# Kernel tuning notes

Hardware: AMD Instinct MI355X
Metric: run time of the kernel (lower is better)

Reference implementation:

```python
import jax, jax.numpy as jnp
import numpy as np

BATCH = 65536
SEQ_LEN = 32
EMB = 64
H = 128


def setup_inputs() -> dict:
    key = jax.random.key(0)
    ks = jax.random.split(key, 12)
    s = 0.05
    inp = {
        "last_pos": jax.random.normal(ks[0], (BATCH, 2), jnp.float32),
        "last_pos_rel": jax.random.normal(ks[1], (BATCH, 2), jnp.float32),
        "hh": jax.random.normal(ks[2], (1, BATCH, H), jnp.float32),
        "ch": jax.random.normal(ks[3], (1, BATCH, H), jnp.float32),
        "seq_start_end": jnp.sort(jax.random.randint(ks[4], (256, 2), 0, BATCH), axis=0),
        # LSTM(embedding_dim -> h_dim), PyTorch gate order [i, f, g, o]
        "w_ih": jax.random.normal(ks[5], (4 * H, EMB), jnp.float32) * s,
        "w_hh": jax.random.normal(ks[6], (4 * H, H), jnp.float32) * s,
        "b_ih": jax.random.normal(ks[7], (4 * H,), jnp.float32) * s,
        "b_hh": jax.random.normal(ks[8], (4 * H,), jnp.float32) * s,
        # spatial_embedding: Linear(2 -> EMB)
        "w_emb": jax.random.normal(ks[9], (EMB, 2), jnp.float32) * s,
        "b_emb": jax.random.normal(ks[10], (EMB,), jnp.float32) * s,
        # hidden2pos: Linear(H -> 2)
        "w_pos": jax.random.normal(ks[11], (2, H), jnp.float32) * s,
        "b_pos": jnp.zeros((2,), jnp.float32),
    }
    return inp


def _decode(last_pos, last_pos_rel, hh, ch, w_ih, w_hh, b_ih, b_hh,
            w_emb, b_emb, w_pos, b_pos):
    h0, c0 = hh[0], ch[0]                      # (B, H)
    x0 = last_pos_rel @ w_emb.T + b_emb        # (B, EMB)
    b = b_ih + b_hh

    def step(carry, _):
        h, c, lp, x = carry
        gates = x @ w_ih.T + h @ w_hh.T + b    # (B, 4H)
        i, f, g, o = jnp.split(gates, 4, axis=-1)
        c2 = jax.nn.sigmoid(f) * c + jax.nn.sigmoid(i) * jnp.tanh(g)
        h2 = jax.nn.sigmoid(o) * jnp.tanh(c2)
        rel = h2 @ w_pos.T + b_pos             # (B, 2)
        cur = rel + lp
        x2 = rel @ w_emb.T + b_emb             # next decoder input embedding
        return (h2, c2, cur, x2), rel

    (hN, cN, _, _), rels = jax.lax.scan(step, (h0, c0, last_pos, x0),
                                        None, length=SEQ_LEN)
    # rels: (SEQ_LEN, B, 2) == pred_traj_fake_rel; hN[None]: (1, B, H)
    return rels, hN[None]


def reference(last_pos, last_pos_rel, hh, ch, seq_start_end,
              w_ih, w_hh, b_ih, b_hh, w_emb, b_emb, w_pos, b_pos):
    # seq_start_end is unused when pool_every_timestep=False
    return _decode(last_pos, last_pos_rel, hh, ch,
                   w_ih, w_hh, b_ih, b_hh, w_emb, b_emb, w_pos, b_pos)
```

## Files before the change

kernel.cpp:

```cpp
#include <hip/hip_runtime.h>

#define B_TOT 65536
#define SEQ   32

typedef __bf16 bf16_8 __attribute__((ext_vector_type(8)));
typedef float  float4v __attribute__((ext_vector_type(4)));

__device__ inline float bf2f(unsigned short s){
    unsigned u = ((unsigned)s) << 16;
    return __builtin_bit_cast(float, u);
}
__device__ inline unsigned short f2bf(float f){
    unsigned u = __builtin_bit_cast(unsigned, f);
    u += 0x7FFFu + ((u >> 16) & 1u);
    return (unsigned short)(u >> 16);
}
__device__ inline float fsig(float x){
    float e = __builtin_amdgcn_exp2f(-1.4426950408889634f * x);
    return __builtin_amdgcn_rcpf(1.0f + e);
}
__device__ inline float ftanh(float x){
    float e = __builtin_amdgcn_exp2f(-2.8853900817779268f * x);
    return 2.0f * __builtin_amdgcn_rcpf(1.0f + e) - 1.0f;
}

__global__ void prep_kernel(const float* __restrict__ w_ih,
                            const float* __restrict__ w_hh,
                            const float* __restrict__ b_ih,
                            const float* __restrict__ b_hh,
                            const float* __restrict__ w_emb,
                            const float* __restrict__ b_emb,
                            const float* __restrict__ w_pos,
                            const float* __restrict__ b_pos,
                            unsigned short* __restrict__ weff,
                            float* __restrict__ beff,
                            float* __restrict__ m2,
                            unsigned short* __restrict__ wposb)
{
    int n = threadIdx.x;
    float m20 = 0.f, m21 = 0.f, bi = 0.f;
    for (int e = 0; e < 64; ++e){
        float wv = w_ih[n*64 + e];
        m20 += w_emb[e*2 + 0] * wv;
        m21 += w_emb[e*2 + 1] * wv;
        bi  += b_emb[e] * wv;
    }
    m2[n]       = m20;
    m2[512 + n] = m21;
    beff[n] = b_ih[n] + b_hh[n] + bi + b_pos[0]*m20 + b_pos[1]*m21;
    for (int k = 0; k < 128; ++k){
        float wv = w_hh[n*128 + k] + w_pos[k]*m20 + w_pos[128 + k]*m21;
        weff[n*128 + k] = f2bf(wv);
    }
    if (n < 256) wposb[n] = f2bf(w_pos[n]);
}

__global__ __launch_bounds__(256, 2) void dec_kernel(
    const float* __restrict__ lpr,
    const float* __restrict__ hh,
    const float* __restrict__ ch,
    const float* __restrict__ b_pos,
    const unsigned short* __restrict__ wposb,
    const unsigned short* __restrict__ weff,
    const float* __restrict__ beff,
    const float* __restrict__ m2,
    float* __restrict__ out)
{
    __shared__ __align__(16) unsigned short lh[2][16][136];
    __shared__ float ubuf[16][2];

    const int tid  = threadIdx.x;
    const int w    = tid >> 6;
    const int lane = tid & 63;
    const int q    = lane >> 4;
    const int l    = lane & 15;
    const int row0 = blockIdx.x << 4;

    {
        int r = tid >> 4, c8 = (tid & 15) << 3;
        const float* ph = hh + ((row0 + r) << 7) + c8;
        const float* pc = ch + ((row0 + r) << 7) + c8;
        float4 h0v = *(const float4*)ph, h1v = *(const float4*)(ph + 4);
        float4 c0v = *(const float4*)pc, c1v = *(const float4*)(pc + 4);
        unsigned short hb[8], cb[8];
        hb[0]=f2bf(h0v.x); hb[1]=f2bf(h0v.y); hb[2]=f2bf(h0v.z); hb[3]=f2bf(h0v.w);
        hb[4]=f2bf(h1v.x); hb[5]=f2bf(h1v.y); hb[6]=f2bf(h1v.z); hb[7]=f2bf(h1v.w);
        cb[0]=f2bf(c0v.x); cb[1]=f2bf(c0v.y); cb[2]=f2bf(c0v.z); cb[3]=f2bf(c0v.w);
        cb[4]=f2bf(c1v.x); cb[5]=f2bf(c1v.y); cb[6]=f2bf(c1v.z); cb[7]=f2bf(c1v.w);
        *(uint4*)&lh[0][r][c8] = *(const uint4*)hb;
        *(uint4*)&lh[1][r][c8] = *(const uint4*)cb;
    }
    __syncthreads();

    float c0r[4], c1r[4];
#pragma unroll
    for (int r4 = 0; r4 < 4; ++r4){
        c0r[r4] = bf2f(lh[1][q*4 + r4][32*w + l]);
        c1r[r4] = bf2f(lh[1][q*4 + r4][32*w + 16 + l]);
    }

    bf16_8 a[4];
#pragma unroll
    for (int kt = 0; kt < 4; ++kt)
        a[kt] = *(const bf16_8*)&lh[0][l][kt*32 + q*8];

    bf16_8 bfr[8][4];
    float bias[8];
#pragma unroll
    for (int t8 = 0; t8 < 8; ++t8){
        int nb = ((t8 >> 1) << 7) + 32*w + ((t8 & 1) << 4) + l;
#pragma unroll
        for (int kt = 0; kt < 4; ++kt)
            bfr[t8][kt] = *(const bf16_8*)(weff + (nb << 7) + kt*32 + q*8);
        bias[t8] = beff[nb];
    }

    bf16_8 wp[4];
    {
        int n2 = (l < 2) ? l : 0;
#pragma unroll
        for (int kt = 0; kt < 4; ++kt)
            wp[kt] = *(const bf16_8*)(wposb + (n2 << 7) + kt*32 + q*8);
    }
    float bposv = b_pos[l & 1];

    if (w == 0){
        float4v racc = {0.f, 0.f, 0.f, 0.f};
#pragma unroll
        for (int kt = 0; kt < 4; ++kt)
            racc = __builtin_amdgcn_mfma_f32_16x16x32_bf16(a[kt], wp[kt], racc, 0, 0, 0);
        if (l < 2){
#pragma unroll
            for (int r4 = 0; r4 < 4; ++r4){
                int row = q*4 + r4;
                float lp = lpr[((row0 + row) << 1) + l];
                ubuf[row][l] = lp - (racc[r4] + bposv);
            }
        }
    }
    __syncthreads();

    float4v acc[8];

    auto do_gates = [&](){
#pragma unroll
        for (int t8 = 0; t8 < 8; ++t8){
            float bb = bias[t8];
            acc[t8] = (float4v){bb, bb, bb, bb};
        }
#pragma unroll
        for (int kt = 0; kt < 4; ++kt)
#pragma unroll
            for (int t8 = 0; t8 < 8; ++t8)
                acc[t8] = __builtin_amdgcn_mfma_f32_16x16x32_bf16(a[kt], bfr[t8][kt], acc[t8], 0, 0, 0);
    };

    auto do_elem_write = [&](int buf, int final_h){
#pragma unroll
        for (int X = 0; X < 2; ++X){
#pragma unroll
            for (int r4 = 0; r4 < 4; ++r4){
                float ig = acc[0 + X][r4];
                float fg = acc[2 + X][r4];
                float gg = acc[4 + X][r4];
                float og = acc[6 + X][r4];
                float cold = X ? c1r[r4] : c0r[r4];
                float c2 = fsig(fg)*cold + fsig(ig)*ftanh(gg);
                float h2 = fsig(og)*ftanh(c2);
                if (X) c1r[r4] = c2; else c0r[r4] = c2;
                lh[buf][q*4 + r4][32*w + 16*X + l] = f2bf(h2);
                if (final_h)
                    out[SEQ*B_TOT*2 + ((row0 + q*4 + r4) << 7) + 32*w + 16*X + l] = h2;
            }
        }
    };

    auto reload_and_rel = [&](int buf, int t){
#pragma unroll
        for (int kt = 0; kt < 4; ++kt)
            a[kt] = *(const bf16_8*)&lh[buf][l][kt*32 + q*8];
        if (w == 0){
            float4v racc = {0.f, 0.f, 0.f, 0.f};
#pragma unroll
            for (int kt = 0; kt < 4; ++kt)
                racc = __builtin_amdgcn_mfma_f32_16x16x32_bf16(a[kt], wp[kt], racc, 0, 0, 0);
            if (l < 2){
#pragma unroll
                for (int r4 = 0; r4 < 4; ++r4)
                    out[t*(B_TOT*2) + ((row0 + q*4 + r4) << 1) + l] = racc[r4] + bposv;
            }
        }
    };

    do_gates();
    {
        float uu0[4], uu1[4];
#pragma unroll
        for (int r4 = 0; r4 < 4; ++r4){
            uu0[r4] = ubuf[q*4 + r4][0];
            uu1[r4] = ubuf[q*4 + r4][1];
        }
#pragma unroll
        for (int t8 = 0; t8 < 8; ++t8){
            int nb = ((t8 >> 1) << 7) + 32*w + ((t8 & 1) << 4) + l;
            float ma = m2[nb], mb = m2[512 + nb];
#pragma unroll
            for (int r4 = 0; r4 < 4; ++r4)
                acc[t8][r4] += uu0[r4]*ma + uu1[r4]*mb;
        }
    }
    do_elem_write(1, 0);
    __syncthreads();
    reload_and_rel(1, 0);

    for (int t = 1; t < SEQ; ++t){
        do_gates();
        do_elem_write((t + 1) & 1, t == SEQ - 1);
        __syncthreads();
        reload_and_rel((t + 1) & 1, t);
    }
}

extern "C" void kernel_launch(void* const* d_in, const int* in_sizes, int n_in,
                              void* d_out, int out_size, void* d_ws, size_t ws_size,
                              hipStream_t stream)
{
    (void)in_sizes; (void)n_in; (void)out_size; (void)ws_size;

    const float* lpr   = (const float*)d_in[1];
    const float* hh    = (const float*)d_in[2];
    const float* ch    = (const float*)d_in[3];
    const float* w_ih  = (const float*)d_in[5];
    const float* w_hh  = (const float*)d_in[6];
    const float* b_ih  = (const float*)d_in[7];
    const float* b_hh  = (const float*)d_in[8];
    const float* w_emb = (const float*)d_in[9];
    const float* b_emb = (const float*)d_in[10];
    const float* w_pos = (const float*)d_in[11];
    const float* b_pos = (const float*)d_in[12];

    unsigned short* weff  = (unsigned short*)d_ws;
    float* beff           = (float*)((char*)d_ws + 512*128*2);
    float* m2             = (float*)((char*)d_ws + 512*128*2 + 2048);
    unsigned short* wposb = (unsigned short*)((char*)d_ws + 512*128*2 + 2048 + 4096);

    hipLaunchKernelGGL(prep_kernel, dim3(1), dim3(512), 0, stream,
                       w_ih, w_hh, b_ih, b_hh, w_emb, b_emb, w_pos, b_pos,
                       weff, beff, m2, wposb);
    hipLaunchKernelGGL(dec_kernel, dim3(B_TOT/16), dim3(256), 0, stream,
                       lpr, hh, ch, b_pos, wposb, weff, beff, m2,
                       (float*)d_out);
}
```

Measured before the change: 549.2 us.

## Transpose MFMA operands so gates are computed as W·hᵀ with vectorized state I/O

Swaps the MFMA operand roles so weights are the A operand and the hidden state is the B operand. Each lane then owns four consecutive gate outputs for one batch row, which allows vectorized bf16x4 LDS writes of h, float4 reads of c and final h, and bias loaded as a float4 accumulator init. The initial LDS staging of h/c and the extra barrier are removed, and the hidden2pos projection rotates across waves per timestep instead of always running on wave 0. The w_pos buffer is zero-padded to 16 rows to serve as the MFMA A operand.

```diff
diff --git a/kernel.cpp b/kernel.cpp
--- a/kernel.cpp
+++ b/kernel.cpp
@@ -4,12 +4,10 @@
 #define SEQ   32
 
 typedef __bf16 bf16_8 __attribute__((ext_vector_type(8)));
+typedef __bf16 bf16_4 __attribute__((ext_vector_type(4)));
 typedef float  float4v __attribute__((ext_vector_type(4)));
-
-__device__ inline float bf2f(unsigned short s){
-    unsigned u = ((unsigned)s) << 16;
-    return __builtin_bit_cast(float, u);
-}
+typedef float  float2v __attribute__((ext_vector_type(2)));
+
 __device__ inline unsigned short f2bf(float f){
     unsigned u = __builtin_bit_cast(unsigned, f);
     u += 0x7FFFu + ((u >> 16) & 1u);
@@ -35,7 +33,7 @@
                             unsigned short* __restrict__ weff,
                             float* __restrict__ beff,
                             float* __restrict__ m2,
-                            unsigned short* __restrict__ wposb)
+                            unsigned short* __restrict__ wposA)
 {
     int n = threadIdx.x;
     float m20 = 0.f, m21 = 0.f, bi = 0.f;
@@ -52,7 +50,8 @@
         float wv = w_hh[n*128 + k] + w_pos[k]*m20 + w_pos[128 + k]*m21;
         weff[n*128 + k] = f2bf(wv);
     }
-    if (n < 256) wposb[n] = f2bf(w_pos[n]);
+    if (n < 256) wposA[n] = f2bf(w_pos[n]);
+    for (int idx = n; idx < 14*128; idx += 512) wposA[256 + idx] = 0;
 }
 
 __global__ __launch_bounds__(256, 2) void dec_kernel(
@@ -60,7 +59,7 @@
     const float* __restrict__ hh,
     const float* __restrict__ ch,
     const float* __restrict__ b_pos,
-    const unsigned short* __restrict__ wposb,
+    const unsigned short* __restrict__ wposA,
     const unsigned short* __restrict__ weff,
     const float* __restrict__ beff,
     const float* __restrict__ m2,
@@ -75,141 +74,124 @@
     const int q    = lane >> 4;
     const int l    = lane & 15;
     const int row0 = blockIdx.x << 4;
-
-    {
-        int r = tid >> 4, c8 = (tid & 15) << 3;
-        const float* ph = hh + ((row0 + r) << 7) + c8;
-        const float* pc = ch + ((row0 + r) << 7) + c8;
-        float4 h0v = *(const float4*)ph, h1v = *(const float4*)(ph + 4);
-        float4 c0v = *(const float4*)pc, c1v = *(const float4*)(pc + 4);
-        unsigned short hb[8], cb[8];
-        hb[0]=f2bf(h0v.x); hb[1]=f2bf(h0v.y); hb[2]=f2bf(h0v.z); hb[3]=f2bf(h0v.w);
-        hb[4]=f2bf(h1v.x); hb[5]=f2bf(h1v.y); hb[6]=f2bf(h1v.z); hb[7]=f2bf(h1v.w);
-        cb[0]=f2bf(c0v.x); cb[1]=f2bf(c0v.y); cb[2]=f2bf(c0v.z); cb[3]=f2bf(c0v.w);
-        cb[4]=f2bf(c1v.x); cb[5]=f2bf(c1v.y); cb[6]=f2bf(c1v.z); cb[7]=f2bf(c1v.w);
-        *(uint4*)&lh[0][r][c8] = *(const uint4*)hb;
-        *(uint4*)&lh[1][r][c8] = *(const uint4*)cb;
+    const int batch = row0 + l;
+
+    bf16_8 wA[8][4];
+    float4v bias4[8];
+#pragma unroll
+    for (int t8 = 0; t8 < 8; ++t8){
+        int nbase = ((t8 >> 1) << 7) + 32*w + ((t8 & 1) << 4);
+        int gA = nbase + l;
+#pragma unroll
+        for (int kt = 0; kt < 4; ++kt)
+            wA[t8][kt] = *(const bf16_8*)(weff + (gA << 7) + kt*32 + (q << 3));
+        bias4[t8] = *(const float4v*)(beff + nbase + (q << 2));
+    }
+
+    bf16_8 wpA[4];
+#pragma unroll
+    for (int kt = 0; kt < 4; ++kt)
+        wpA[kt] = *(const bf16_8*)(wposA + (l << 7) + kt*32 + (q << 3));
+    const float bp0 = b_pos[0], bp1 = b_pos[1];
+
+    float4v cst[2];
+#pragma unroll
+    for (int X = 0; X < 2; ++X)
+        cst[X] = *(const float4v*)(ch + (batch << 7) + 32*w + 16*X + (q << 2));
+
+    bf16_8 b[4];
+#pragma unroll
+    for (int kt = 0; kt < 4; ++kt){
+        const float* ph = hh + (batch << 7) + kt*32 + (q << 3);
+        float4v h0 = *(const float4v*)ph;
+        float4v h1 = *(const float4v*)(ph + 4);
+        bf16_8 t;
+        t[0]=(__bf16)h0[0]; t[1]=(__bf16)h0[1]; t[2]=(__bf16)h0[2]; t[3]=(__bf16)h0[3];
+        t[4]=(__bf16)h1[0]; t[5]=(__bf16)h1[1]; t[6]=(__bf16)h1[2]; t[7]=(__bf16)h1[3];
+        b[kt] = t;
+    }
+
+    if (w == 0){
+        float4v r = {0.f, 0.f, 0.f, 0.f};
+#pragma unroll
+        for (int kt = 0; kt < 4; ++kt)
+            r = __builtin_amdgcn_mfma_f32_16x16x32_bf16(wpA[kt], b[kt], r, 0, 0, 0);
+        if (q == 0){
+            float2v lp = *(const float2v*)(lpr + (batch << 1));
+            ubuf[l][0] = lp[0] - (r[0] + bp0);
+            ubuf[l][1] = lp[1] - (r[1] + bp1);
+        }
     }
     __syncthreads();
 
-    float c0r[4], c1r[4];
-#pragma unroll
-    for (int r4 = 0; r4 < 4; ++r4){
-        c0r[r4] = bf2f(lh[1][q*4 + r4][32*w + l]);
-        c1r[r4] = bf2f(lh[1][q*4 + r4][32*w + 16 + l]);
-    }
-
-    bf16_8 a[4];
-#pragma unroll
-    for (int kt = 0; kt < 4; ++kt)
-        a[kt] = *(const bf16_8*)&lh[0][l][kt*32 + q*8];
-
-    bf16_8 bfr[8][4];
-    float bias[8];
-#pragma unroll
-    for (int t8 = 0; t8 < 8; ++t8){
-        int nb = ((t8 >> 1) << 7) + 32*w + ((t8 & 1) << 4) + l;
-#pragma unroll
-        for (int kt = 0; kt < 4; ++kt)
-            bfr[t8][kt] = *(const bf16_8*)(weff + (nb << 7) + kt*32 + q*8);
-        bias[t8] = beff[nb];
-    }
-
-    bf16_8 wp[4];
-    {
-        int n2 = (l < 2) ? l : 0;
-#pragma unroll
-        for (int kt = 0; kt < 4; ++kt)
-            wp[kt] = *(const bf16_8*)(wposb + (n2 << 7) + kt*32 + q*8);
-    }
-    float bposv = b_pos[l & 1];
-
-    if (w == 0){
-        float4v racc = {0.f, 0.f, 0.f, 0.f};
-#pragma unroll
-        for (int kt = 0; kt < 4; ++kt)
-            racc = __builtin_amdgcn_mfma_f32_16x16x32_bf16(a[kt], wp[kt], racc, 0, 0, 0);
-        if (l < 2){
-#pragma unroll
-            for (int r4 = 0; r4 < 4; ++r4){
-                int row = q*4 + r4;
-                float lp = lpr[((row0 + row) << 1) + l];
-                ubuf[row][l] = lp - (racc[r4] + bposv);
-            }
-        }
-    }
-    __syncthreads();
-
     float4v acc[8];
 
     auto do_gates = [&](){
 #pragma unroll
-        for (int t8 = 0; t8 < 8; ++t8){
-            float bb = bias[t8];
-            acc[t8] = (float4v){bb, bb, bb, bb};
-        }
-#pragma unroll
-        for (int kt = 0; kt < 4; ++kt)
+        for (int t8 = 0; t8 < 8; ++t8)
+            acc[t8] = __builtin_amdgcn_mfma_f32_16x16x32_bf16(wA[t8][0], b[0], bias4[t8], 0, 0, 0);
+#pragma unroll
+        for (int kt = 1; kt < 4; ++kt)
 #pragma unroll
             for (int t8 = 0; t8 < 8; ++t8)
-                acc[t8] = __builtin_amdgcn_mfma_f32_16x16x32_bf16(a[kt], bfr[t8][kt], acc[t8], 0, 0, 0);
+                acc[t8] = __builtin_amdgcn_mfma_f32_16x16x32_bf16(wA[t8][kt], b[kt], acc[t8], 0, 0, 0);
     };
 
-    auto do_elem_write = [&](int buf, int final_h){
+    auto do_elem_write = [&](int buf, bool finalh){
 #pragma unroll
         for (int X = 0; X < 2; ++X){
+            bf16_4 hv;
+            float4v hf;
 #pragma unroll
             for (int r4 = 0; r4 < 4; ++r4){
                 float ig = acc[0 + X][r4];
                 float fg = acc[2 + X][r4];
                 float gg = acc[4 + X][r4];
                 float og = acc[6 + X][r4];
-                float cold = X ? c1r[r4] : c0r[r4];
-                float c2 = fsig(fg)*cold + fsig(ig)*ftanh(gg);
+                float c2 = fsig(fg)*cst[X][r4] + fsig(ig)*ftanh(gg);
                 float h2 = fsig(og)*ftanh(c2);
-                if (X) c1r[r4] = c2; else c0r[r4] = c2;
-                lh[buf][q*4 + r4][32*w + 16*X + l] = f2bf(h2);
-                if (final_h)
-                    out[SEQ*B_TOT*2 + ((row0 + q*4 + r4) << 7) + 32*w + 16*X + l] = h2;
+                cst[X][r4] = c2;
+                hv[r4] = (__bf16)h2;
+                hf[r4] = h2;
             }
+            *(bf16_4*)&lh[buf][l][32*w + 16*X + (q << 2)] = hv;
+            if (finalh)
+                *(float4v*)(out + SEQ*B_TOT*2 + (batch << 7) + 32*w + 16*X + (q << 2)) = hf;
         }
     };
 
     auto reload_and_rel = [&](int buf, int t){
 #pragma unroll
         for (int kt = 0; kt < 4; ++kt)
-            a[kt] = *(const bf16_8*)&lh[buf][l][kt*32 + q*8];
-        if (w == 0){
-            float4v racc = {0.f, 0.f, 0.f, 0.f};
+            b[kt] = *(const bf16_8*)&lh[buf][l][kt*32 + (q << 3)];
+        if (w == (t & 3)){
+            float4v r = {0.f, 0.f, 0.f, 0.f};
 #pragma unroll
             for (int kt = 0; kt < 4; ++kt)
-                racc = __builtin_amdgcn_mfma_f32_16x16x32_bf16(a[kt], wp[kt], racc, 0, 0, 0);
-            if (l < 2){
-#pragma unroll
-                for (int r4 = 0; r4 < 4; ++r4)
-                    out[t*(B_TOT*2) + ((row0 + q*4 + r4) << 1) + l] = racc[r4] + bposv;
+                r = __builtin_amdgcn_mfma_f32_16x16x32_bf16(wpA[kt], b[kt], r, 0, 0, 0);
+            if (q == 0){
+                float2v rv;
+                rv[0] = r[0] + bp0;
+                rv[1] = r[1] + bp1;
+                *(float2v*)(out + t*(B_TOT*2) + (batch << 1)) = rv;
             }
         }
     };
 
     do_gates();
     {
-        float uu0[4], uu1[4];
-#pragma unroll
-        for (int r4 = 0; r4 < 4; ++r4){
-            uu0[r4] = ubuf[q*4 + r4][0];
-            uu1[r4] = ubuf[q*4 + r4][1];
-        }
+        float u0 = ubuf[l][0], u1 = ubuf[l][1];
 #pragma unroll
         for (int t8 = 0; t8 < 8; ++t8){
-            int nb = ((t8 >> 1) << 7) + 32*w + ((t8 & 1) << 4) + l;
-            float ma = m2[nb], mb = m2[512 + nb];
+            int g0 = ((t8 >> 1) << 7) + 32*w + ((t8 & 1) << 4) + (q << 2);
+            float4v ma = *(const float4v*)(m2 + g0);
+            float4v mb = *(const float4v*)(m2 + 512 + g0);
 #pragma unroll
             for (int r4 = 0; r4 < 4; ++r4)
-                acc[t8][r4] += uu0[r4]*ma + uu1[r4]*mb;
-        }
-    }
-    do_elem_write(1, 0);
+                acc[t8][r4] += u0*ma[r4] + u1*mb[r4];
+        }
+    }
+    do_elem_write(1, false);
     __syncthreads();
     reload_and_rel(1, 0);
 
@@ -240,14 +222,14 @@
     const float* b_pos = (const float*)d_in[12];
 
     unsigned short* weff  = (unsigned short*)d_ws;
-    float* beff           = (float*)((char*)d_ws + 512*128*2);
-    float* m2             = (float*)((char*)d_ws + 512*128*2 + 2048);
-    unsigned short* wposb = (unsigned short*)((char*)d_ws + 512*128*2 + 2048 + 4096);
+    float* beff           = (float*)((char*)d_ws + 131072);
+    float* m2             = (float*)((char*)d_ws + 131072 + 2048);
+    unsigned short* wposA = (unsigned short*)((char*)d_ws + 131072 + 2048 + 4096);
 
     hipLaunchKernelGGL(prep_kernel, dim3(1), dim3(512), 0, stream,
                        w_ih, w_hh, b_ih, b_hh, w_emb, b_emb, w_pos, b_pos,
-                       weff, beff, m2, wposb);
+                       weff, beff, m2, wposA);
     hipLaunchKernelGGL(dec_kernel, dim3(B_TOT/16), dim3(256), 0, stream,
-                       lpr, hh, ch, b_pos, wposb, weff, beff, m2,
+                       lpr, hh, ch, b_pos, wposA, weff, beff, m2,
                        (float*)d_out);
 }
```

Measured after the change: 545.5 us. No clear change (-0.7%).
